# Performance work log

Hardware: AMD Instinct MI355X
Metric: run time of the kernel (lower is better)

## Reference

```python
import jax, jax.numpy as jnp
import numpy as np

N_NODES = 20000
N_EDGES = 320000
IN_F = 256
HID = 64
OUT_F = 64
EDGE_F = 16
HEADS = 4
NUM_CLASSES = 10
NUM_GRAPHS = 40
ALPHA = 0.2  # LeakyReLU negative slope


def _xavier(key, shape):
    fan_in, fan_out = shape[0], shape[-1]
    std = 1.414 * np.sqrt(2.0 / (fan_in + fan_out))
    return jax.random.normal(key, shape, dtype=jnp.float32) * std


def setup_inputs() -> dict:
    key = jax.random.key(0)
    ks = jax.random.split(key, 12)
    x = jax.random.normal(ks[0], (N_NODES, IN_F), dtype=jnp.float32)
    edge_index = jax.random.randint(ks[1], (2, N_EDGES), 0, N_NODES, dtype=jnp.int32)
    edge_attr = jax.random.uniform(ks[2], (N_EDGES, EDGE_F), dtype=jnp.float32)
    batch = jnp.sort(jax.random.randint(ks[3], (N_NODES,), 0, NUM_GRAPHS, dtype=jnp.int32))
    # layer 0: in=IN_F, heads=HEADS, out=HID, concat
    W0 = _xavier(ks[4], (IN_F, HEADS * HID))
    a0 = _xavier(ks[5], (HEADS, 2 * HID + EDGE_F))
    # layer 1: in=HID*HEADS, heads=HEADS, out=HID, concat
    W1 = _xavier(ks[6], (HID * HEADS, HEADS * HID))
    a1 = _xavier(ks[7], (HEADS, 2 * HID + EDGE_F))
    # layer 2: in=HID*HEADS, heads=1, out=OUT_F, mean over heads
    W2 = _xavier(ks[8], (HID * HEADS, 1 * OUT_F))
    a2 = _xavier(ks[9], (1, 2 * OUT_F + EDGE_F))
    cls_w = _xavier(ks[10], (OUT_F, NUM_CLASSES))
    cls_b = jnp.zeros((NUM_CLASSES,), dtype=jnp.float32)
    return {"x": x, "edge_index": edge_index, "edge_attr": edge_attr, "batch": batch,
            "W0": W0, "a0": a0, "W1": W1, "a1": a1, "W2": W2, "a2": a2,
            "cls_w": cls_w, "cls_b": cls_b}


def gat_layer(h, W, a, edge_index, edge_attr, heads, out_f, concat):
    n = h.shape[0]
    Wh = (h @ W).reshape(n, heads, out_f)              # [N,H,D]
    src, dst = edge_index[0], edge_index[1]
    a_i, a_j, a_e = a[:, :out_f], a[:, out_f:2 * out_f], a[:, 2 * out_f:]
    # per-node head scores, gathered per edge (equivalent to concat + dot with a)
    s_i = jnp.einsum('nhd,hd->nh', Wh, a_i)            # [N,H]
    s_j = jnp.einsum('nhd,hd->nh', Wh, a_j)            # [N,H]
    s_e = edge_attr @ a_e.T                            # [E,H]
    e = s_i[src] + s_j[dst] + s_e                      # [E,H]
    e = jnp.where(e > 0, e, ALPHA * e)                 # LeakyReLU
    # NB: faithful to source — softmax over the HEADS dim (dim=1), not per-node
    att = jax.nn.softmax(e, axis=1)                    # [E,H]
    msg = att[:, :, None] * Wh[dst]                    # [E,H,D]
    h_prime = jax.ops.segment_sum(msg, src, num_segments=n)  # scatter-add to src
    if concat:
        return jax.nn.elu(h_prime.reshape(n, heads * out_f))
    return h_prime.mean(axis=1)


def reference(x, edge_index, edge_attr, batch, W0, a0, W1, a1, W2, a2, cls_w, cls_b):
    h = gat_layer(x, W0, a0, edge_index, edge_attr, HEADS, HID, True)
    h = gat_layer(h, W1, a1, edge_index, edge_attr, HEADS, HID, True)
    h = gat_layer(h, W2, a2, edge_index, edge_attr, 1, OUT_F, False)
    # global mean pool over graphs
    sums = jax.ops.segment_sum(h, batch, num_segments=NUM_GRAPHS)
    cnts = jax.ops.segment_sum(jnp.ones((h.shape[0],), h.dtype), batch, num_segments=NUM_GRAPHS)
    pooled = sums / jnp.maximum(cnts, 1.0)[:, None]
    logits = pooled @ cls_w + cls_b
    return jax.nn.log_softmax(logits, axis=1)
```

## Files before the change

### kernel.cpp

```cpp
#include <hip/hip_runtime.h>
#include <hip/hip_bf16.h>
#include <math.h>

#define N_NODES 20000
#define N_EDGES 320000
#define IN_F 256
#define HID 64
#define HEADS 4
#define OUT_F 64
#define EDGE_F 16
#define NUM_CLASSES 10
#define NUM_GRAPHS 40
#define LRELU_ALPHA 0.2f

typedef short bf16x8 __attribute__((ext_vector_type(8)));
typedef unsigned short u16x8 __attribute__((ext_vector_type(8)));
typedef float f32x4 __attribute__((ext_vector_type(4)));

static __device__ __forceinline__ float bf2f(unsigned short u) {
    union { unsigned int i; float f; } v; v.i = ((unsigned int)u) << 16; return v.f;
}
static __device__ __forceinline__ unsigned short f2bf(float f) {
    union { float f; unsigned int i; } v; v.f = f;
    unsigned int r = v.i + 0x7FFF + ((v.i >> 16) & 1);
    return (unsigned short)(r >> 16);
}
static __device__ __forceinline__ float eluf(float a) {
    return a > 0.f ? a : __expf(a) - 1.0f;
}

__global__ void prep_kernel(const float* __restrict__ W0, const float* __restrict__ W1,
                            const float* __restrict__ W2, unsigned short* __restrict__ W0b,
                            unsigned short* __restrict__ W1b, unsigned short* __restrict__ W2b,
                            int* __restrict__ cnt) {
    int b = blockIdx.x;
    if (b < 144) {
        int i = b * 256 + threadIdx.x;
        const float* src; unsigned short* dst; int off;
        if (i < 16384)      { src = W0; dst = W0b; off = i; }
        else if (i < 32768) { src = W1; dst = W1b; off = i - 16384; }
        else                { src = W2; dst = W2b; off = i - 32768; }
        float4 v = ((const float4*)src)[off];
        ushort4 o;
        o.x = f2bf(v.x); o.y = f2bf(v.y); o.z = f2bf(v.z); o.w = f2bf(v.w);
        ((ushort4*)dst)[off] = o;
    } else {
        int j = (b - 144) * 256 + threadIdx.x;
        if (j < N_NODES / 4) ((int4*)cnt)[j] = make_int4(0, 0, 0, 0);
    }
}

__global__ void count_kernel(const int4* __restrict__ src4, int* __restrict__ cnt) {
    int i = blockIdx.x * blockDim.x + threadIdx.x;
    if (i < N_EDGES / 4) {
        int4 s = src4[i];
        atomicAdd(&cnt[s.x], 1);
        atomicAdd(&cnt[s.y], 1);
        atomicAdd(&cnt[s.z], 1);
        atomicAdd(&cnt[s.w], 1);
    }
}

__global__ __launch_bounds__(1024) void scan_kernel(const int* __restrict__ cnt,
                                                    int* __restrict__ row_ptr,
                                                    int* __restrict__ cursor) {
    __shared__ int wsum[16];
    __shared__ int carry_s;
    int t = threadIdx.x;
    int lane = t & 63, wave = t >> 6;
    if (t == 0) { carry_s = 0; row_ptr[0] = 0; }
    __syncthreads();
    for (int base = 0; base < N_NODES; base += 1024) {
        int idx = base + t;
        int x0 = (idx < N_NODES) ? cnt[idx] : 0;
        int x = x0;
#pragma unroll
        for (int off = 1; off < 64; off <<= 1) {
            int y = __shfl_up(x, off, 64);
            if (lane >= off) x += y;
        }
        if (lane == 63) wsum[wave] = x;
        __syncthreads();
        if (wave == 0 && lane < 16) {
            int s = wsum[lane];
#pragma unroll
            for (int off = 1; off < 16; off <<= 1) {
                int y = __shfl_up(s, off, 64);
                if (lane >= off) s += y;
            }
            wsum[lane] = s;
        }
        __syncthreads();
        int waveoff = (wave > 0) ? wsum[wave - 1] : 0;
        int carry = carry_s;
        if (idx < N_NODES) {
            int incl = x + waveoff + carry;
            row_ptr[idx + 1] = incl;
            cursor[idx] = incl - x0;
        }
        __syncthreads();
        if (t == 0) carry_s = carry + wsum[15];
        __syncthreads();
    }
}

__global__ void scatter_kernel(const int* __restrict__ src, const int* __restrict__ dst,
                               int* __restrict__ cursor, int* __restrict__ dstp,
                               int* __restrict__ eperm) {
    int e = blockIdx.x * blockDim.x + threadIdx.x;
    if (e < N_EDGES) {
        int s = src[e];
        int pos = atomicAdd(&cursor[s], 1);
        dstp[pos] = dst[e];
        eperm[e] = pos;
    }
}

template <bool AF32, bool SCORES>
__global__ __launch_bounds__(256) void gemm_bf16(const void* __restrict__ Aptr,
                                                 const unsigned short* __restrict__ B,
                                                 unsigned short* __restrict__ C,
                                                 const float* __restrict__ avec,
                                                 float* __restrict__ si, float* __restrict__ sj,
                                                 int M, int N, int K) {
    __shared__ unsigned short As[128][40];
    __shared__ unsigned short Bs[64][40];
    __shared__ unsigned short Cs[128][72];
    __shared__ float sa[128];
    int tid = threadIdx.x;
    if (SCORES && tid < 128) sa[tid] = avec[blockIdx.y * 144 + tid];
    int bm = blockIdx.x * 128, bn = blockIdx.y * 64;
    int w = tid >> 6, l = tid & 63;
    int wr = w * 32;
    int lr = l & 15, lk = (l >> 4) * 8;
    f32x4 acc[2][4] = {};
    int ar = tid >> 1, akc = (tid & 1) * 16;
    int bk = tid >> 3, bn8 = tid & 7, bnc = bn8 * 8;

    for (int k0 = 0; k0 < K; k0 += 32) {
        bf16x8 av0 = {}, av1 = {};
        if (bm + ar < M) {
            if constexpr (AF32) {
                const float* Af = (const float*)Aptr + (size_t)(bm + ar) * K + k0 + akc;
                float4 f0 = ((const float4*)Af)[0];
                float4 f1 = ((const float4*)Af)[1];
                float4 f2 = ((const float4*)Af)[2];
                float4 f3 = ((const float4*)Af)[3];
                av0[0] = (short)f2bf(f0.x); av0[1] = (short)f2bf(f0.y);
                av0[2] = (short)f2bf(f0.z); av0[3] = (short)f2bf(f0.w);
                av0[4] = (short)f2bf(f1.x); av0[5] = (short)f2bf(f1.y);
                av0[6] = (short)f2bf(f1.z); av0[7] = (short)f2bf(f1.w);
                av1[0] = (short)f2bf(f2.x); av1[1] = (short)f2bf(f2.y);
                av1[2] = (short)f2bf(f2.z); av1[3] = (short)f2bf(f2.w);
                av1[4] = (short)f2bf(f3.x); av1[5] = (short)f2bf(f3.y);
                av1[6] = (short)f2bf(f3.z); av1[7] = (short)f2bf(f3.w);
            } else {
                const unsigned short* Ab = (const unsigned short*)Aptr + (size_t)(bm + ar) * K + k0 + akc;
                av0 = *(const bf16x8*)Ab;
                av1 = *(const bf16x8*)(Ab + 8);
            }
        }
        *(bf16x8*)&As[ar][akc] = av0;
        *(bf16x8*)&As[ar][akc + 8] = av1;
        bf16x8 bv = *(const bf16x8*)(B + (size_t)(k0 + bk) * N + bn + bnc);
#pragma unroll
        for (int j = 0; j < 8; ++j) {
            int jj = (j + bn8) & 7;
            Bs[bnc + jj][bk] = (unsigned short)bv[jj];
        }
        __syncthreads();
        bf16x8 a0 = *(const bf16x8*)&As[wr + lr][lk];
        bf16x8 a1 = *(const bf16x8*)&As[wr + 16 + lr][lk];
        bf16x8 b0 = *(const bf16x8*)&Bs[lr][lk];
        bf16x8 b1 = *(const bf16x8*)&Bs[16 + lr][lk];
        bf16x8 b2 = *(const bf16x8*)&Bs[32 + lr][lk];
        bf16x8 b3 = *(const bf16x8*)&Bs[48 + lr][lk];
        acc[0][0] = __builtin_amdgcn_mfma_f32_16x16x32_bf16(a0, b0, acc[0][0], 0, 0, 0);
        acc[0][1] = __builtin_amdgcn_mfma_f32_16x16x32_bf16(a0, b1, acc[0][1], 0, 0, 0);
        acc[0][2] = __builtin_amdgcn_mfma_f32_16x16x32_bf16(a0, b2, acc[0][2], 0, 0, 0);
        acc[0][3] = __builtin_amdgcn_mfma_f32_16x16x32_bf16(a0, b3, acc[0][3], 0, 0, 0);
        acc[1][0] = __builtin_amdgcn_mfma_f32_16x16x32_bf16(a1, b0, acc[1][0], 0, 0, 0);
        acc[1][1] = __builtin_amdgcn_mfma_f32_16x16x32_bf16(a1, b1, acc[1][1], 0, 0, 0);
        acc[1][2] = __builtin_amdgcn_mfma_f32_16x16x32_bf16(a1, b2, acc[1][2], 0, 0, 0);
        acc[1][3] = __builtin_amdgcn_mfma_f32_16x16x32_bf16(a1, b3, acc[1][3], 0, 0, 0);
        __syncthreads();
    }
#pragma unroll
    for (int i = 0; i < 2; ++i)
#pragma unroll
        for (int j = 0; j < 4; ++j)
#pragma unroll
            for (int r = 0; r < 4; ++r)
                Cs[wr + i * 16 + (l >> 4) * 4 + r][j * 16 + (l & 15)] = f2bf(acc[i][j][r]);
    __syncthreads();
    {
        int row = tid >> 3, cc = (tid & 7) * 8;
#pragma unroll
        for (int p = 0; p < 4; ++p, row += 32) {
            if (bm + row < M) {
                bf16x8 o = *(const bf16x8*)&Cs[row][cc];
                *(bf16x8*)(C + (size_t)(bm + row) * N + bn + cc) = o;
            }
        }
    }
    if (SCORES) {
        int r = tid >> 1, half = tid & 1;
        float s0 = 0.f, s1 = 0.f;
#pragma unroll
        for (int k = 0; k < 32; ++k) {
            float f = bf2f(Cs[r][half * 32 + k]);
            s0 += f * sa[half * 32 + k];
            s1 += f * sa[64 + half * 32 + k];
        }
        s0 += __shfl_xor(s0, 1, 64);
        s1 += __shfl_xor(s1, 1, 64);
        if (half == 0 && bm + r < M) {
            si[(size_t)(bm + r) * 4 + blockIdx.y] = s0;
            sj[(size_t)(bm + r) * 4 + blockIdx.y] = s1;
        }
    }
}

__global__ void att_kernel(const int* __restrict__ src, const int* __restrict__ dst,
                           const float* __restrict__ ea, const float* __restrict__ avec,
                           const float* __restrict__ si, const float* __restrict__ sj,
                           const int* __restrict__ eperm, float4* __restrict__ attp) {
    __shared__ float ae[4][16];
    int tid = threadIdx.x;
    if (tid < 64) ae[tid >> 4][tid & 15] = avec[(tid >> 4) * 144 + 128 + (tid & 15)];
    __syncthreads();
    int e = blockIdx.x * blockDim.x + tid;
    if (e >= N_EDGES) return;
    int s = src[e], u = dst[e];
    float4 siv = ((const float4*)si)[s];
    float4 sjv = ((const float4*)sj)[u];
    float x[16];
#pragma unroll
    for (int k = 0; k < 16; k += 4) {
        float4 v = *(const float4*)(ea + (size_t)e * 16 + k);
        x[k] = v.x; x[k + 1] = v.y; x[k + 2] = v.z; x[k + 3] = v.w;
    }
    float se0 = 0.f, se1 = 0.f, se2 = 0.f, se3 = 0.f;
#pragma unroll
    for (int k = 0; k < 16; ++k) {
        se0 += x[k] * ae[0][k];
        se1 += x[k] * ae[1][k];
        se2 += x[k] * ae[2][k];
        se3 += x[k] * ae[3][k];
    }
    float t0 = siv.x + sjv.x + se0;
    float t1 = siv.y + sjv.y + se1;
    float t2 = siv.z + sjv.z + se2;
    float t3 = siv.w + sjv.w + se3;
    t0 = t0 > 0.f ? t0 : LRELU_ALPHA * t0;
    t1 = t1 > 0.f ? t1 : LRELU_ALPHA * t1;
    t2 = t2 > 0.f ? t2 : LRELU_ALPHA * t2;
    t3 = t3 > 0.f ? t3 : LRELU_ALPHA * t3;
    float m = fmaxf(fmaxf(t0, t1), fmaxf(t2, t3));
    float p0 = __expf(t0 - m), p1 = __expf(t1 - m), p2 = __expf(t2 - m), p3 = __expf(t3 - m);
    float inv = 1.0f / (p0 + p1 + p2 + p3);
    attp[eperm[e]] = make_float4(p0 * inv, p1 * inv, p2 * inv, p3 * inv);
}

__global__ __launch_bounds__(256) void edge_agg_concat(
    const unsigned short* __restrict__ Whb, const float4* __restrict__ attp,
    const int* __restrict__ row_ptr, const int* __restrict__ dstp,
    unsigned short* __restrict__ out) {
    int v = blockIdx.x * 4 + (threadIdx.x >> 6);
    if (v >= N_NODES) return;
    int l = threadIdx.x & 63;
    int slot = l >> 4, p = l & 15;
    int beg = row_ptr[v], end = row_ptr[v + 1];
    float acc0[8] = {}, acc1[8] = {};
    int i = beg + slot;
    int u_n = 0;
    float4 at_n = make_float4(0.f, 0.f, 0.f, 0.f);
    if (i < end) { u_n = dstp[i]; at_n = attp[i]; }
    for (; i < end; i += 4) {
        int u = u_n;
        float4 at4 = at_n;
        if (i + 4 < end) { u_n = dstp[i + 4]; at_n = attp[i + 4]; }
        const unsigned short* row = Whb + (size_t)u * 256;
        u16x8 w0 = *(const u16x8*)(row + p * 8);
        u16x8 w1 = *(const u16x8*)(row + 128 + p * 8);
        float atA = (p & 8) ? at4.y : at4.x;
        float atB = (p & 8) ? at4.w : at4.z;
#pragma unroll
        for (int j = 0; j < 8; ++j) acc0[j] += atA * bf2f(w0[j]);
#pragma unroll
        for (int j = 0; j < 8; ++j) acc1[j] += atB * bf2f(w1[j]);
    }
#pragma unroll
    for (int j = 0; j < 8; ++j) {
        acc0[j] += __shfl_xor(acc0[j], 16, 64);
        acc0[j] += __shfl_xor(acc0[j], 32, 64);
        acc1[j] += __shfl_xor(acc1[j], 16, 64);
        acc1[j] += __shfl_xor(acc1[j], 32, 64);
    }
    if (slot == 0) {
        u16x8 o0, o1;
#pragma unroll
        for (int j = 0; j < 8; ++j) {
            o0[j] = f2bf(eluf(acc0[j]));
            o1[j] = f2bf(eluf(acc1[j]));
        }
        *(u16x8*)(out + (size_t)v * 256 + p * 8) = o0;
        *(u16x8*)(out + (size_t)v * 256 + 128 + p * 8) = o1;
    }
}

__global__ __launch_bounds__(256) void edge_agg_single(
    const unsigned short* __restrict__ Whb, const int* __restrict__ row_ptr,
    const int* __restrict__ dstp, float* __restrict__ out) {
    int v = blockIdx.x * 4 + (threadIdx.x >> 6);
    if (v >= N_NODES) return;
    int l = threadIdx.x & 63;
    int slot = l >> 3, p = l & 7;
    int beg = row_ptr[v], end = row_ptr[v + 1];
    float acc[8] = {};
    int i = beg + slot;
    int u_n = 0;
    if (i < end) u_n = dstp[i];
    for (; i < end; i += 8) {
        int u = u_n;
        if (i + 8 < end) u_n = dstp[i + 8];
        u16x8 w = *(const u16x8*)(Whb + (size_t)u * 64 + p * 8);
#pragma unroll
        for (int j = 0; j < 8; ++j) acc[j] += bf2f(w[j]);
    }
#pragma unroll
    for (int j = 0; j < 8; ++j) {
        acc[j] += __shfl_xor(acc[j], 8, 64);
        acc[j] += __shfl_xor(acc[j], 16, 64);
        acc[j] += __shfl_xor(acc[j], 32, 64);
    }
    if (l < 8) {
        float4 o0 = make_float4(acc[0], acc[1], acc[2], acc[3]);
        float4 o1 = make_float4(acc[4], acc[5], acc[6], acc[7]);
        *(float4*)(out + (size_t)v * 64 + p * 8) = o0;
        *(float4*)(out + (size_t)v * 64 + p * 8 + 4) = o1;
    }
}

__global__ __launch_bounds__(1024) void pool_kernel(const float* __restrict__ h3,
                                                    const int* __restrict__ batch,
                                                    float* __restrict__ pooled) {
    int g = blockIdx.x;
    int lane = threadIdx.x & 63;
    int wave = threadIdx.x >> 6;
    int lo = 0, hi = N_NODES;
    while (lo < hi) { int mid = (lo + hi) >> 1; if (batch[mid] < g) lo = mid + 1; else hi = mid; }
    int start = lo;
    lo = start; hi = N_NODES;
    while (lo < hi) { int mid = (lo + hi) >> 1; if (batch[mid] < g + 1) lo = mid + 1; else hi = mid; }
    int endi = lo;
    float s = 0.f;
    for (int v = start + wave; v < endi; v += 16) s += h3[(size_t)v * 64 + lane];
    __shared__ float red[16][64];
    red[wave][lane] = s;
    __syncthreads();
    if (wave == 0) {
        float t = red[0][lane];
#pragma unroll
        for (int w = 1; w < 16; ++w) t += red[w][lane];
        float c = (float)((endi - start) > 1 ? (endi - start) : 1);
        pooled[g * 64 + lane] = t / c;
    }
}

__global__ void classify_kernel(const float* __restrict__ pooled, const float* __restrict__ cw,
                                const float* __restrict__ cb, float* __restrict__ out) {
    int g = threadIdx.x;
    if (g >= NUM_GRAPHS) return;
    float lg[NUM_CLASSES];
#pragma unroll
    for (int c = 0; c < NUM_CLASSES; ++c) lg[c] = cb[c];
    for (int d = 0; d < OUT_F; ++d) {
        float p = pooled[g * 64 + d];
#pragma unroll
        for (int c = 0; c < NUM_CLASSES; ++c) lg[c] += p * cw[d * NUM_CLASSES + c];
    }
    float m = lg[0];
#pragma unroll
    for (int c = 1; c < NUM_CLASSES; ++c) m = fmaxf(m, lg[c]);
    float s = 0.f;
#pragma unroll
    for (int c = 0; c < NUM_CLASSES; ++c) s += expf(lg[c] - m);
    float lse = m + logf(s);
#pragma unroll
    for (int c = 0; c < NUM_CLASSES; ++c) out[g * NUM_CLASSES + c] = lg[c] - lse;
}

extern "C" void kernel_launch(void* const* d_in, const int* in_sizes, int n_in,
                              void* d_out, int out_size, void* d_ws, size_t ws_size,
                              hipStream_t stream) {
    const float* x   = (const float*)d_in[0];
    const int*   ei  = (const int*)d_in[1];
    const float* ea  = (const float*)d_in[2];
    const int* batch = (const int*)d_in[3];
    const float* W0  = (const float*)d_in[4];
    const float* a0  = (const float*)d_in[5];
    const float* W1  = (const float*)d_in[6];
    const float* a1  = (const float*)d_in[7];
    const float* W2  = (const float*)d_in[8];
    const float* cw  = (const float*)d_in[10];
    const float* cb  = (const float*)d_in[11];
    float* out = (float*)d_out;

    const int* srcg = ei;
    const int* dstg = ei + N_EDGES;

    char* ws = (char*)d_ws;
    size_t off = 0;
    auto alloc = [&](size_t bytes) -> char* {
        char* p = ws + off;
        off += (bytes + 255) & ~(size_t)255;
        return p;
    };
    unsigned short* W0b  = (unsigned short*)alloc(256 * 256 * 2);
    unsigned short* W1b  = (unsigned short*)alloc(256 * 256 * 2);
    unsigned short* W2b  = (unsigned short*)alloc(256 * 64 * 2);
    unsigned short* Whb  = (unsigned short*)alloc((size_t)N_NODES * 256 * 2);
    unsigned short* hAb  = (unsigned short*)alloc((size_t)N_NODES * 256 * 2);
    unsigned short* hBb  = (unsigned short*)alloc((size_t)N_NODES * 256 * 2);
    unsigned short* Wh2b = (unsigned short*)alloc((size_t)N_NODES * 64 * 2);
    float* si   = (float*)alloc((size_t)N_NODES * HEADS * 4);
    float* sj   = (float*)alloc((size_t)N_NODES * HEADS * 4);
    float* attp = (float*)alloc((size_t)N_EDGES * HEADS * 4);
    int* row_ptr = (int*)alloc((N_NODES + 1) * 4);
    int* cursor  = (int*)alloc(N_NODES * 4);
    int* cnt  = (int*)alloc(N_NODES * 4);
    int* dstp = (int*)alloc(N_EDGES * 4);
    int* eperm = (int*)alloc(N_EDGES * 4);
    float* h3 = (float*)alloc((size_t)N_NODES * 64 * 4);
    float* pooled = (float*)alloc(NUM_GRAPHS * 64 * 4);

    prep_kernel<<<144 + (N_NODES / 4 + 255) / 256, 256, 0, stream>>>(W0, W1, W2, W0b, W1b, W2b, cnt);

    count_kernel<<<(N_EDGES / 4 + 255) / 256, 256, 0, stream>>>((const int4*)srcg, cnt);
    scan_kernel<<<1, 1024, 0, stream>>>(cnt, row_ptr, cursor);
    scatter_kernel<<<(N_EDGES + 255) / 256, 256, 0, stream>>>(srcg, dstg, cursor, dstp, eperm);

    dim3 ggrid((N_NODES + 127) / 128, 4);
    dim3 ggrid2((N_NODES + 127) / 128, 1);
    int atb = (N_EDGES + 255) / 256;
    int agb = (N_NODES + 3) / 4;

    gemm_bf16<true, true><<<ggrid, 256, 0, stream>>>(x, W0b, Whb, a0, si, sj, N_NODES, 256, 256);
    att_kernel<<<atb, 256, 0, stream>>>(srcg, dstg, ea, a0, si, sj, eperm, (float4*)attp);
    edge_agg_concat<<<agb, 256, 0, stream>>>(Whb, (const float4*)attp, row_ptr, dstp, hAb);

    gemm_bf16<false, true><<<ggrid, 256, 0, stream>>>(hAb, W1b, Whb, a1, si, sj, N_NODES, 256, 256);
    att_kernel<<<atb, 256, 0, stream>>>(srcg, dstg, ea, a1, si, sj, eperm, (float4*)attp);
    edge_agg_concat<<<agb, 256, 0, stream>>>(Whb, (const float4*)attp, row_ptr, dstp, hBb);

    gemm_bf16<false, false><<<ggrid2, 256, 0, stream>>>(hBb, W2b, Wh2b, nullptr, nullptr, nullptr,
                                                        N_NODES, 64, 256);
    edge_agg_single<<<agb, 256, 0, stream>>>(Wh2b, row_ptr, dstp, h3);

    pool_kernel<<<NUM_GRAPHS, 1024, 0, stream>>>(h3, batch, pooled);
    classify_kernel<<<1, 64, 0, stream>>>(pooled, cw, cb, out);
}
```

Measured before the change: 211.0 us.

## Use 128x128 GEMM tiles with pretransposed weights and register prefetch; invert edge permutation

The weight matrices for layers 0 and 1 are now transposed to bf16 in the prep kernel, so the GEMM can load B tiles with vector stores instead of scattered transposes. The GEMM tile grows from 128x64 to 128x128, with each warp computing a 64x64 sub-tile, and the next K slice is prefetched into registers while the current one is computed. This halves the passes over A and adds reuse, at the cost of more registers and a two-phase epilogue that fuses the per-head score computation. The attention kernel now writes in original edge order, and the aggregation reads through a pos->edge permutation, making the writes coalesced but the reads indirect.

Result: slower. 217.8 us (+3.2%).

```diff
diff --git a/kernel.cpp b/kernel.cpp
--- a/kernel.cpp
+++ b/kernel.cpp
@@ -30,22 +30,42 @@
 }
 
 __global__ void prep_kernel(const float* __restrict__ W0, const float* __restrict__ W1,
-                            const float* __restrict__ W2, unsigned short* __restrict__ W0b,
-                            unsigned short* __restrict__ W1b, unsigned short* __restrict__ W2b,
+                            const float* __restrict__ W2, unsigned short* __restrict__ W0t,
+                            unsigned short* __restrict__ W1t, unsigned short* __restrict__ W2b,
                             int* __restrict__ cnt) {
-    int b = blockIdx.x;
-    if (b < 144) {
-        int i = b * 256 + threadIdx.x;
-        const float* src; unsigned short* dst; int off;
-        if (i < 16384)      { src = W0; dst = W0b; off = i; }
-        else if (i < 32768) { src = W1; dst = W1b; off = i - 16384; }
-        else                { src = W2; dst = W2b; off = i - 32768; }
-        float4 v = ((const float4*)src)[off];
+    int b = blockIdx.x, t = threadIdx.x;
+    if (b < 32) {
+        __shared__ unsigned short tl[64][65];
+        const float* W = (b < 16) ? W0 : W1;
+        unsigned short* Wt = (b < 16) ? W0t : W1t;
+        int tile = b & 15;
+        int tk = (tile >> 2) * 64, tn = (tile & 3) * 64;
+        int kl = t >> 2, cg = (t & 3) * 16;
+        const float* sp = W + (size_t)(tk + kl) * 256 + tn + cg;
+#pragma unroll
+        for (int q = 0; q < 4; ++q) {
+            float4 v = ((const float4*)sp)[q];
+            tl[kl][cg + q * 4 + 0] = f2bf(v.x);
+            tl[kl][cg + q * 4 + 1] = f2bf(v.y);
+            tl[kl][cg + q * 4 + 2] = f2bf(v.z);
+            tl[kl][cg + q * 4 + 3] = f2bf(v.w);
+        }
+        __syncthreads();
+        int nl = t >> 2, kg = (t & 3) * 16;
+        u16x8 o0, o1;
+#pragma unroll
+        for (int q = 0; q < 8; ++q) { o0[q] = tl[kg + q][nl]; o1[q] = tl[kg + 8 + q][nl]; }
+        unsigned short* dst = Wt + (size_t)(tn + nl) * 256 + tk + kg;
+        *(u16x8*)dst = o0;
+        *(u16x8*)(dst + 8) = o1;
+    } else if (b < 48) {
+        int i = (b - 32) * 256 + t;
+        float4 v = ((const float4*)W2)[i];
         ushort4 o;
         o.x = f2bf(v.x); o.y = f2bf(v.y); o.z = f2bf(v.z); o.w = f2bf(v.w);
-        ((ushort4*)dst)[off] = o;
+        ((ushort4*)W2b)[i] = o;
     } else {
-        int j = (b - 144) * 256 + threadIdx.x;
+        int j = (b - 48) * 256 + t;
         if (j < N_NODES / 4) ((int4*)cnt)[j] = make_int4(0, 0, 0, 0);
     }
 }
@@ -106,30 +126,145 @@
 
 __global__ void scatter_kernel(const int* __restrict__ src, const int* __restrict__ dst,
                                int* __restrict__ cursor, int* __restrict__ dstp,
-                               int* __restrict__ eperm) {
+                               int* __restrict__ perm) {
     int e = blockIdx.x * blockDim.x + threadIdx.x;
     if (e < N_EDGES) {
         int s = src[e];
         int pos = atomicAdd(&cursor[s], 1);
         dstp[pos] = dst[e];
-        eperm[e] = pos;
+        perm[pos] = e;
     }
 }
 
 template <bool AF32, bool SCORES>
-__global__ __launch_bounds__(256) void gemm_bf16(const void* __restrict__ Aptr,
-                                                 const unsigned short* __restrict__ B,
-                                                 unsigned short* __restrict__ C,
-                                                 const float* __restrict__ avec,
-                                                 float* __restrict__ si, float* __restrict__ sj,
-                                                 int M, int N, int K) {
+__global__ __launch_bounds__(256) void gemm128(const void* __restrict__ Aptr,
+                                               const unsigned short* __restrict__ Bt,
+                                               unsigned short* __restrict__ C,
+                                               const float* __restrict__ avec,
+                                               float* __restrict__ si, float* __restrict__ sj,
+                                               int M) {
+    __shared__ unsigned short smem[2 * 128 * 40];
+    __shared__ float sa[2][128];
+    unsigned short (*As)[40] = (unsigned short(*)[40])smem;
+    unsigned short (*Bs)[40] = (unsigned short(*)[40])(smem + 128 * 40);
+    unsigned short (*Cs)[136] = (unsigned short(*)[136])smem;
+    int tid = threadIdx.x;
+    int bm = blockIdx.x * 128, bn = blockIdx.y * 128;
+    if (SCORES) {
+        int hh = tid >> 7, idx = tid & 127;
+        sa[hh][idx] = avec[((bn >> 6) + hh) * 144 + idx];
+    }
+    int w = tid >> 6, l = tid & 63;
+    int wr = (w >> 1) * 64, wc = (w & 1) * 64;
+    int lr = l & 15, lk = (l >> 4) * 8;
+    f32x4 acc[4][4] = {};
+    int srow = tid >> 1, skc = (tid & 1) * 16;
+    bool arow_ok = (bm + srow < M);
+    const float* Af32 = (const float*)Aptr + (size_t)(bm + srow) * 256 + skc;
+    const unsigned short* Ab16 = (const unsigned short*)Aptr + (size_t)(bm + srow) * 256 + skc;
+    const unsigned short* Bb = Bt + (size_t)(bn + srow) * 256 + skc;
+
+    bf16x8 av0 = {}, av1 = {}, bv0, bv1;
+    if (arow_ok) {
+        if constexpr (AF32) {
+            float4 f0 = ((const float4*)Af32)[0], f1 = ((const float4*)Af32)[1];
+            float4 f2 = ((const float4*)Af32)[2], f3 = ((const float4*)Af32)[3];
+            av0[0]=(short)f2bf(f0.x); av0[1]=(short)f2bf(f0.y); av0[2]=(short)f2bf(f0.z); av0[3]=(short)f2bf(f0.w);
+            av0[4]=(short)f2bf(f1.x); av0[5]=(short)f2bf(f1.y); av0[6]=(short)f2bf(f1.z); av0[7]=(short)f2bf(f1.w);
+            av1[0]=(short)f2bf(f2.x); av1[1]=(short)f2bf(f2.y); av1[2]=(short)f2bf(f2.z); av1[3]=(short)f2bf(f2.w);
+            av1[4]=(short)f2bf(f3.x); av1[5]=(short)f2bf(f3.y); av1[6]=(short)f2bf(f3.z); av1[7]=(short)f2bf(f3.w);
+        } else {
+            av0 = *(const bf16x8*)(Ab16);
+            av1 = *(const bf16x8*)(Ab16 + 8);
+        }
+    }
+    bv0 = *(const bf16x8*)(Bb);
+    bv1 = *(const bf16x8*)(Bb + 8);
+
+    for (int k0 = 0; k0 < 256; k0 += 32) {
+        *(bf16x8*)&As[srow][skc] = av0;
+        *(bf16x8*)&As[srow][skc + 8] = av1;
+        *(bf16x8*)&Bs[srow][skc] = bv0;
+        *(bf16x8*)&Bs[srow][skc + 8] = bv1;
+        if (k0 + 32 < 256) {
+            if (arow_ok) {
+                if constexpr (AF32) {
+                    const float* p = Af32 + k0 + 32;
+                    float4 f0 = ((const float4*)p)[0], f1 = ((const float4*)p)[1];
+                    float4 f2 = ((const float4*)p)[2], f3 = ((const float4*)p)[3];
+                    av0[0]=(short)f2bf(f0.x); av0[1]=(short)f2bf(f0.y); av0[2]=(short)f2bf(f0.z); av0[3]=(short)f2bf(f0.w);
+                    av0[4]=(short)f2bf(f1.x); av0[5]=(short)f2bf(f1.y); av0[6]=(short)f2bf(f1.z); av0[7]=(short)f2bf(f1.w);
+                    av1[0]=(short)f2bf(f2.x); av1[1]=(short)f2bf(f2.y); av1[2]=(short)f2bf(f2.z); av1[3]=(short)f2bf(f2.w);
+                    av1[4]=(short)f2bf(f3.x); av1[5]=(short)f2bf(f3.y); av1[6]=(short)f2bf(f3.z); av1[7]=(short)f2bf(f3.w);
+                } else {
+                    av0 = *(const bf16x8*)(Ab16 + k0 + 32);
+                    av1 = *(const bf16x8*)(Ab16 + k0 + 40);
+                }
+            }
+            bv0 = *(const bf16x8*)(Bb + k0 + 32);
+            bv1 = *(const bf16x8*)(Bb + k0 + 40);
+        }
+        __syncthreads();
+        bf16x8 af[4], bfr[4];
+#pragma unroll
+        for (int i = 0; i < 4; ++i) af[i] = *(const bf16x8*)&As[wr + i * 16 + lr][lk];
+#pragma unroll
+        for (int j = 0; j < 4; ++j) bfr[j] = *(const bf16x8*)&Bs[wc + j * 16 + lr][lk];
+#pragma unroll
+        for (int i = 0; i < 4; ++i)
+#pragma unroll
+            for (int j = 0; j < 4; ++j)
+                acc[i][j] = __builtin_amdgcn_mfma_f32_16x16x32_bf16(af[i], bfr[j], acc[i][j], 0, 0, 0);
+        __syncthreads();
+    }
+
+#pragma unroll
+    for (int h = 0; h < 2; ++h) {
+        if ((w >> 1) == h) {
+#pragma unroll
+            for (int i = 0; i < 4; ++i)
+#pragma unroll
+                for (int j = 0; j < 4; ++j)
+#pragma unroll
+                    for (int r = 0; r < 4; ++r)
+                        Cs[i * 16 + (l >> 4) * 4 + r][wc + j * 16 + lr] = f2bf(acc[i][j][r]);
+        }
+        __syncthreads();
+        int row = tid >> 2;
+        int grow = bm + h * 64 + row;
+        if (grow < M) {
+            int c0 = (tid & 3) * 8;
+#pragma unroll
+            for (int q = 0; q < 4; ++q) {
+                bf16x8 o = *(const bf16x8*)&Cs[row][c0 + q * 32];
+                *(bf16x8*)(C + (size_t)grow * 256 + bn + c0 + q * 32) = o;
+            }
+        }
+        if (SCORES) {
+            int q = tid & 3, hl = q >> 1, sel = q & 1;
+            float s = 0.f;
+#pragma unroll
+            for (int c = 0; c < 64; ++c)
+                s += bf2f(Cs[row][hl * 64 + c]) * sa[hl][sel * 64 + c];
+            if (grow < M) {
+                int head = (bn >> 6) + hl;
+                if (sel == 0) si[(size_t)grow * 4 + head] = s;
+                else          sj[(size_t)grow * 4 + head] = s;
+            }
+        }
+        __syncthreads();
+    }
+}
+
+__global__ __launch_bounds__(256) void gemm64(const unsigned short* __restrict__ Aptr,
+                                              const unsigned short* __restrict__ B,
+                                              unsigned short* __restrict__ C,
+                                              int M, int N, int K) {
     __shared__ unsigned short As[128][40];
     __shared__ unsigned short Bs[64][40];
     __shared__ unsigned short Cs[128][72];
-    __shared__ float sa[128];
     int tid = threadIdx.x;
-    if (SCORES && tid < 128) sa[tid] = avec[blockIdx.y * 144 + tid];
-    int bm = blockIdx.x * 128, bn = blockIdx.y * 64;
+    int bm = blockIdx.x * 128, bn = 0;
     int w = tid >> 6, l = tid & 63;
     int wr = w * 32;
     int lr = l & 15, lk = (l >> 4) * 8;
@@ -140,25 +275,9 @@
     for (int k0 = 0; k0 < K; k0 += 32) {
         bf16x8 av0 = {}, av1 = {};
         if (bm + ar < M) {
-            if constexpr (AF32) {
-                const float* Af = (const float*)Aptr + (size_t)(bm + ar) * K + k0 + akc;
-                float4 f0 = ((const float4*)Af)[0];
-                float4 f1 = ((const float4*)Af)[1];
-                float4 f2 = ((const float4*)Af)[2];
-                float4 f3 = ((const float4*)Af)[3];
-                av0[0] = (short)f2bf(f0.x); av0[1] = (short)f2bf(f0.y);
-                av0[2] = (short)f2bf(f0.z); av0[3] = (short)f2bf(f0.w);
-                av0[4] = (short)f2bf(f1.x); av0[5] = (short)f2bf(f1.y);
-                av0[6] = (short)f2bf(f1.z); av0[7] = (short)f2bf(f1.w);
-                av1[0] = (short)f2bf(f2.x); av1[1] = (short)f2bf(f2.y);
-                av1[2] = (short)f2bf(f2.z); av1[3] = (short)f2bf(f2.w);
-                av1[4] = (short)f2bf(f3.x); av1[5] = (short)f2bf(f3.y);
-                av1[6] = (short)f2bf(f3.z); av1[7] = (short)f2bf(f3.w);
-            } else {
-                const unsigned short* Ab = (const unsigned short*)Aptr + (size_t)(bm + ar) * K + k0 + akc;
-                av0 = *(const bf16x8*)Ab;
-                av1 = *(const bf16x8*)(Ab + 8);
-            }
+            const unsigned short* Ab = Aptr + (size_t)(bm + ar) * K + k0 + akc;
+            av0 = *(const bf16x8*)Ab;
+            av1 = *(const bf16x8*)(Ab + 8);
         }
         *(bf16x8*)&As[ar][akc] = av0;
         *(bf16x8*)&As[ar][akc + 8] = av1;
@@ -193,30 +312,12 @@
             for (int r = 0; r < 4; ++r)
                 Cs[wr + i * 16 + (l >> 4) * 4 + r][j * 16 + (l & 15)] = f2bf(acc[i][j][r]);
     __syncthreads();
-    {
-        int row = tid >> 3, cc = (tid & 7) * 8;
-#pragma unroll
-        for (int p = 0; p < 4; ++p, row += 32) {
-            if (bm + row < M) {
-                bf16x8 o = *(const bf16x8*)&Cs[row][cc];
-                *(bf16x8*)(C + (size_t)(bm + row) * N + bn + cc) = o;
-            }
-        }
-    }
-    if (SCORES) {
-        int r = tid >> 1, half = tid & 1;
-        float s0 = 0.f, s1 = 0.f;
-#pragma unroll
-        for (int k = 0; k < 32; ++k) {
-            float f = bf2f(Cs[r][half * 32 + k]);
-            s0 += f * sa[half * 32 + k];
-            s1 += f * sa[64 + half * 32 + k];
-        }
-        s0 += __shfl_xor(s0, 1, 64);
-        s1 += __shfl_xor(s1, 1, 64);
-        if (half == 0 && bm + r < M) {
-            si[(size_t)(bm + r) * 4 + blockIdx.y] = s0;
-            sj[(size_t)(bm + r) * 4 + blockIdx.y] = s1;
+    int row = tid >> 3, cc = (tid & 7) * 8;
+#pragma unroll
+    for (int p = 0; p < 4; ++p, row += 32) {
+        if (bm + row < M) {
+            bf16x8 o = *(const bf16x8*)&Cs[row][cc];
+            *(bf16x8*)(C + (size_t)(bm + row) * N + cc) = o;
         }
     }
 }
@@ -224,7 +325,7 @@
 __global__ void att_kernel(const int* __restrict__ src, const int* __restrict__ dst,
                            const float* __restrict__ ea, const float* __restrict__ avec,
                            const float* __restrict__ si, const float* __restrict__ sj,
-                           const int* __restrict__ eperm, float4* __restrict__ attp) {
+                           float4* __restrict__ attp) {
     __shared__ float ae[4][16];
     int tid = threadIdx.x;
     if (tid < 64) ae[tid >> 4][tid & 15] = avec[(tid >> 4) * 144 + 128 + (tid & 15)];
@@ -259,13 +360,13 @@
     float m = fmaxf(fmaxf(t0, t1), fmaxf(t2, t3));
     float p0 = __expf(t0 - m), p1 = __expf(t1 - m), p2 = __expf(t2 - m), p3 = __expf(t3 - m);
     float inv = 1.0f / (p0 + p1 + p2 + p3);
-    attp[eperm[e]] = make_float4(p0 * inv, p1 * inv, p2 * inv, p3 * inv);
+    attp[e] = make_float4(p0 * inv, p1 * inv, p2 * inv, p3 * inv);
 }
 
 __global__ __launch_bounds__(256) void edge_agg_concat(
     const unsigned short* __restrict__ Whb, const float4* __restrict__ attp,
     const int* __restrict__ row_ptr, const int* __restrict__ dstp,
-    unsigned short* __restrict__ out) {
+    const int* __restrict__ perm, unsigned short* __restrict__ out) {
     int v = blockIdx.x * 4 + (threadIdx.x >> 6);
     if (v >= N_NODES) return;
     int l = threadIdx.x & 63;
@@ -275,11 +376,11 @@
     int i = beg + slot;
     int u_n = 0;
     float4 at_n = make_float4(0.f, 0.f, 0.f, 0.f);
-    if (i < end) { u_n = dstp[i]; at_n = attp[i]; }
+    if (i < end) { u_n = dstp[i]; at_n = attp[perm[i]]; }
     for (; i < end; i += 4) {
         int u = u_n;
         float4 at4 = at_n;
-        if (i + 4 < end) { u_n = dstp[i + 4]; at_n = attp[i + 4]; }
+        if (i + 4 < end) { u_n = dstp[i + 4]; at_n = attp[perm[i + 4]]; }
         const unsigned short* row = Whb + (size_t)u * 256;
         u16x8 w0 = *(const u16x8*)(row + p * 8);
         u16x8 w1 = *(const u16x8*)(row + 128 + p * 8);
@@ -417,8 +518,8 @@
         off += (bytes + 255) & ~(size_t)255;
         return p;
     };
-    unsigned short* W0b  = (unsigned short*)alloc(256 * 256 * 2);
-    unsigned short* W1b  = (unsigned short*)alloc(256 * 256 * 2);
+    unsigned short* W0t  = (unsigned short*)alloc(256 * 256 * 2);
+    unsigned short* W1t  = (unsigned short*)alloc(256 * 256 * 2);
     unsigned short* W2b  = (unsigned short*)alloc(256 * 64 * 2);
     unsigned short* Whb  = (unsigned short*)alloc((size_t)N_NODES * 256 * 2);
     unsigned short* hAb  = (unsigned short*)alloc((size_t)N_NODES * 256 * 2);
@@ -431,31 +532,30 @@
     int* cursor  = (int*)alloc(N_NODES * 4);
     int* cnt  = (int*)alloc(N_NODES * 4);
     int* dstp = (int*)alloc(N_EDGES * 4);
-    int* eperm = (int*)alloc(N_EDGES * 4);
+    int* perm = (int*)alloc(N_EDGES * 4);
     float* h3 = (float*)alloc((size_t)N_NODES * 64 * 4);
     float* pooled = (float*)alloc(NUM_GRAPHS * 64 * 4);
 
-    prep_kernel<<<144 + (N_NODES / 4 + 255) / 256, 256, 0, stream>>>(W0, W1, W2, W0b, W1b, W2b, cnt);
+    prep_kernel<<<48 + (N_NODES / 4 + 255) / 256, 256, 0, stream>>>(W0, W1, W2, W0t, W1t, W2b, cnt);
 
     count_kernel<<<(N_EDGES / 4 + 255) / 256, 256, 0, stream>>>((const int4*)srcg, cnt);
     scan_kernel<<<1, 1024, 0, stream>>>(cnt, row_ptr, cursor);
-    scatter_kernel<<<(N_EDGES + 255) / 256, 256, 0, stream>>>(srcg, dstg, cursor, dstp, eperm);
-
-    dim3 ggrid((N_NODES + 127) / 128, 4);
-    dim3 ggrid2((N_NODES + 127) / 128, 1);
+    scatter_kernel<<<(N_EDGES + 255) / 256, 256, 0, stream>>>(srcg, dstg, cursor, dstp, perm);
+
+    dim3 g128((N_NODES + 127) / 128, 2);
+    int g64 = (N_NODES + 127) / 128;
     int atb = (N_EDGES + 255) / 256;
     int agb = (N_NODES + 3) / 4;
 
-    gemm_bf16<true, true><<<ggrid, 256, 0, stream>>>(x, W0b, Whb, a0, si, sj, N_NODES, 256, 256);
-    att_kernel<<<atb, 256, 0, stream>>>(srcg, dstg, ea, a0, si, sj, eperm, (float4*)attp);
-    edge_agg_concat<<<agb, 256, 0, stream>>>(Whb, (const float4*)attp, row_ptr, dstp, hAb);
-
-    gemm_bf16<false, true><<<ggrid, 256, 0, stream>>>(hAb, W1b, Whb, a1, si, sj, N_NODES, 256, 256);
-    att_kernel<<<atb, 256, 0, stream>>>(srcg, dstg, ea, a1, si, sj, eperm, (float4*)attp);
-    edge_agg_concat<<<agb, 256, 0, stream>>>(Whb, (const float4*)attp, row_ptr, dstp, hBb);
-
-    gemm_bf16<false, false><<<ggrid2, 256, 0, stream>>>(hBb, W2b, Wh2b, nullptr, nullptr, nullptr,
-                                                        N_NODES, 64, 256);
+    gemm128<true, true><<<g128, 256, 0, stream>>>(x, W0t, Whb, a0, si, sj, N_NODES);
+    att_kernel<<<atb, 256, 0, stream>>>(srcg, dstg, ea, a0, si, sj, (float4*)attp);
+    edge_agg_concat<<<agb, 256, 0, stream>>>(Whb, (const float4*)attp, row_ptr, dstp, perm, hAb);
+
+    gemm128<false, true><<<g128, 256, 0, stream>>>(hAb, W1t, Whb, a1, si, sj, N_NODES);
+    att_kernel<<<atb, 256, 0, stream>>>(srcg, dstg, ea, a1, si, sj, (float4*)attp);
+    edge_agg_concat<<<agb, 256, 0, stream>>>(Whb, (const float4*)attp, row_ptr, dstp, perm, hBb);
+
+    gemm64<<<g64, 256, 0, stream>>>(hBb, W2b, Wh2b, N_NODES, 64, 256);
     edge_agg_single<<<agb, 256, 0, stream>>>(Wh2b, row_ptr, dstp, h3);
 
     pool_kernel<<<NUM_GRAPHS, 1024, 0, stream>>>(h3, batch, pooled);
```
